# Kernel tuning notes

Hardware: AMD Instinct MI355X
Metric: run time of the kernel (lower is better)

The kernel has to match this reference:

```python
import jax, jax.numpy as jnp
import numpy as np

EPS = 1e-3  # keras LayerNormalization default epsilon


def layer_norm(x, g, b):
    mu = jnp.mean(x, axis=-1, keepdims=True)
    var = jnp.mean(jnp.square(x - mu), axis=-1, keepdims=True)
    return g * (x - mu) / jnp.sqrt(var + EPS) + b


def setup_inputs() -> dict:
    key = jax.random.key(0)
    ks = jax.random.split(key, 16)
    B, S, E, H, F = 2, 4096, 512, 8, 2048
    s_e = 1.0 / np.sqrt(E)
    s_f = 1.0 / np.sqrt(F)
    inp = {
        "x": jax.random.normal(ks[0], (B, S, E), dtype=jnp.float32),
        "WQ": jax.random.normal(ks[1], (E, E), dtype=jnp.float32) * s_e,
        "bQ": jnp.zeros((E,), jnp.float32),
        "WK": jax.random.normal(ks[2], (E, E), dtype=jnp.float32) * s_e,
        "bK": jnp.zeros((E,), jnp.float32),
        "WV": jax.random.normal(ks[3], (E, E), dtype=jnp.float32) * s_e,
        "bV": jnp.zeros((E,), jnp.float32),
        "WO": jax.random.normal(ks[4], (E, E), dtype=jnp.float32) * s_e,
        "bO": jnp.zeros((E,), jnp.float32),
        "W1": jax.random.normal(ks[5], (E, F), dtype=jnp.float32) * s_e,
        "b1": jnp.zeros((F,), jnp.float32),
        "W2": jax.random.normal(ks[6], (F, E), dtype=jnp.float32) * s_f,
        "b2": jnp.zeros((E,), jnp.float32),
        "g1": jnp.ones((E,), jnp.float32),
        "beta1": jnp.zeros((E,), jnp.float32),
        "g2": jnp.ones((E,), jnp.float32),
        "beta2": jnp.zeros((E,), jnp.float32),
        "num_head": 8,
    }
    return inp


def reference(x, WQ, bQ, WK, bK, WV, bV, WO, bO, W1, b1, W2, b2,
              g1, beta1, g2, beta2, num_head):
    B, S, E = x.shape
    H = num_head
    d = E // H
    scale = jnp.sqrt(jnp.asarray(d, jnp.float32))

    q = (x @ WQ + bQ).reshape(B, S, H, d).transpose(0, 2, 1, 3)  # [B,H,S,d]
    k = (x @ WK + bK).reshape(B, S, H, d).transpose(0, 2, 1, 3)
    v = (x @ WV + bV).reshape(B, S, H, d).transpose(0, 2, 1, 3)

    score = jnp.einsum('bhqd,bhkd->bhqk', q, k) / scale  # O(S^2) materialized, as in source
    attn = jax.nn.softmax(score, axis=-1)
    zs = jnp.einsum('bhqk,bhkd->bhqd', attn, v)  # [B,H,S,d]

    # Faithful to source bug: reshape [B,H,S,d] -> [B,S,E] WITHOUT transposing back
    zs = zs.reshape(B, S, E)
    zs = zs @ WO + bO

    z = layer_norm(zs + x, g1, beta1)
    r = jax.nn.relu(z @ W1 + b1) @ W2 + b2
    r = layer_norm(r + z, g2, beta2)
    return r
```

## Files before the change

### kernel.cpp

```cpp
#include <hip/hip_runtime.h>
#include <hip/hip_bf16.h>

typedef unsigned short u16;
typedef __attribute__((ext_vector_type(8))) short bf16x8;
typedef __attribute__((ext_vector_type(4))) float f32x4;
typedef __attribute__((ext_vector_type(16))) float f32x16;

static constexpr int BB = 2;
static constexpr int SS = 4096;
static constexpr int EE = 512;
static constexpr int HH = 8;
static constexpr int DD = 64;
static constexpr int FF = 2048;
static constexpr int NR = BB * SS;
static constexpr int QS = 3 * EE;

#define QSCALE 0.18033688011112042f

__device__ __forceinline__ u16 f2bf(float f) {
  union { float f; unsigned u; } v; v.f = f;
  unsigned r = v.u + 0x7FFFu + ((v.u >> 16) & 1u);
  return (u16)(r >> 16);
}
__device__ __forceinline__ unsigned pack2(float a, float b) {
  return (unsigned)f2bf(a) | ((unsigned)f2bf(b) << 16);
}
__device__ __forceinline__ unsigned cvtpk(float lo, float hi) {
  unsigned r;
  asm("v_cvt_pk_bf16_f32 %0, %1, %2" : "=v"(r) : "v"(lo), "v"(hi));
  return r;
}
__device__ __forceinline__ void perm32swap(unsigned& a, unsigned& b) {
  asm("v_permlane32_swap_b32 %0, %1" : "+v"(a), "+v"(b));
}
__device__ __forceinline__ void gload_lds16(const u16* g, u16* l) {
  __builtin_amdgcn_global_load_lds(
      (const __attribute__((address_space(1))) unsigned*)g,
      (__attribute__((address_space(3))) unsigned*)l, 16, 0, 0);
}

__global__ __launch_bounds__(256) void cvt_bf16(const float* __restrict__ x,
                                                u16* __restrict__ xb, int n) {
  int i = (blockIdx.x * 256 + threadIdx.x) * 8;
  if (i >= n) return;
  float4 a = *(const float4*)(x + i);
  float4 b = *(const float4*)(x + i + 4);
  uint4 u;
  u.x = pack2(a.x, a.y); u.y = pack2(a.z, a.w);
  u.z = pack2(b.x, b.y); u.w = pack2(b.z, b.w);
  *(uint4*)(xb + i) = u;
}

__global__ __launch_bounds__(256) void transp_bf16(const float* __restrict__ W,
                                                   u16* __restrict__ Wt,
                                                   int K, int N) {
  __shared__ float T[64][65];
  const int k0 = blockIdx.x * 64, n0 = blockIdx.y * 64;
  const int t = threadIdx.x;
  const int tn = t & 63, tk = t >> 6;
#pragma unroll
  for (int i = 0; i < 16; ++i) {
    int kk = tk * 16 + i;
    T[kk][tn] = W[(size_t)(k0 + kk) * N + n0 + tn];
  }
  __syncthreads();
#pragma unroll
  for (int i = 0; i < 16; ++i) {
    int nn = tk * 16 + i;
    Wt[(size_t)(n0 + nn) * K + k0 + tn] = f2bf(T[tn][nn]);
  }
}

__global__ __launch_bounds__(256) void transp_v(const u16* __restrict__ qkvb,
                                                u16* __restrict__ vt) {
  __shared__ u16 T[64][72];
  const int s0 = blockIdx.x * 64, c0 = blockIdx.y * 64, b = blockIdx.z;
  const int t = threadIdx.x;
#pragma unroll
  for (int i = 0; i < 2; ++i) {
    int idx = t + i * 256;
    int row = idx >> 3, c8 = idx & 7;
    *(uint4*)(&T[row][c8 * 8]) = *(const uint4*)(
        &qkvb[((size_t)b * SS + s0 + row) * QS + 1024 + c0 + c8 * 8]);
  }
  __syncthreads();
#pragma unroll
  for (int i = 0; i < 2; ++i) {
    int idx = t + i * 256;
    int c = idx >> 3, s8 = idx & 7;
    u16 tmp[8];
#pragma unroll
    for (int j = 0; j < 8; ++j) tmp[j] = T[s8 * 8 + j][c];
    *(uint4*)(&vt[((size_t)b * EE + c0 + c) * SS + s0 + s8 * 8]) =
        *(uint4*)tmp;
  }
}

__global__ void concat_bias(const float* __restrict__ bQ,
                            const float* __restrict__ bK,
                            const float* __restrict__ bV,
                            float* __restrict__ bqkv) {
  int i = blockIdx.x * 256 + threadIdx.x;
  if (i >= QS) return;
  bqkv[i] = i < 512 ? bQ[i] : (i < 1024 ? bK[i - 512] : bV[i - 1024]);
}

template <int RELU, int OUT_BF16, int SCALEQ = 0>
__global__ __launch_bounds__(256) void gemm_mfma(
    const u16* __restrict__ A, const u16* __restrict__ Bt,
    const float* __restrict__ bias, void* __restrict__ Cout,
    int M, int N, int K) {
  __shared__ __align__(16) u16 As[128 * 64];
  __shared__ __align__(16) u16 Bs[128 * 64];
  const int t = threadIdx.x;
  const int lane = t & 63, wid = t >> 6;
  const int lm = lane & 15, lg = lane >> 4;
  const int bm = blockIdx.x * 128, bn = blockIdx.y * 128;
  const int wr = (wid >> 1) * 64, wc = (wid & 1) * 64;
  const int sr = lane >> 3;
  const int scb = (lane & 7) ^ sr;

  f32x4 acc[4][4];
#pragma unroll
  for (int i = 0; i < 4; ++i)
#pragma unroll
    for (int j = 0; j < 4; ++j) acc[i][j] = (f32x4){0.f, 0.f, 0.f, 0.f};

  for (int kb = 0; kb < K; kb += 64) {
    __syncthreads();
#pragma unroll
    for (int i = 0; i < 4; ++i) {
      int rr = wid * 32 + i * 8 + sr;
      gload_lds16(A + (size_t)(bm + rr) * K + kb + scb * 8,
                  &As[(wid * 32 + i * 8) * 64]);
      gload_lds16(Bt + (size_t)(bn + rr) * K + kb + scb * 8,
                  &Bs[(wid * 32 + i * 8) * 64]);
    }
    __syncthreads();

#pragma unroll
    for (int c = 0; c < 2; ++c) {
      bf16x8 af[4], bfr[4];
#pragma unroll
      for (int i = 0; i < 4; ++i) {
        int ar = wr + i * 16 + lm;
        af[i] = *(const bf16x8*)(&As[ar * 64 + (((c * 4 + lg) ^ (ar & 7)) << 3)]);
        int br = wc + i * 16 + lm;
        bfr[i] = *(const bf16x8*)(&Bs[br * 64 + (((c * 4 + lg) ^ (br & 7)) << 3)]);
      }
#pragma unroll
      for (int i = 0; i < 4; ++i)
#pragma unroll
        for (int j = 0; j < 4; ++j)
          acc[i][j] = __builtin_amdgcn_mfma_f32_16x16x32_bf16(
              af[i], bfr[j], acc[i][j], 0, 0, 0);
    }
  }

  float bi[4];
#pragma unroll
  for (int j = 0; j < 4; ++j) bi[j] = bias[bn + wc + j * 16 + lm];

#pragma unroll
  for (int i = 0; i < 4; ++i) {
#pragma unroll
    for (int j = 0; j < 4; ++j) {
      int col = bn + wc + j * 16 + lm;
#pragma unroll
      for (int r = 0; r < 4; ++r) {
        int row = bm + wr + i * 16 + lg * 4 + r;
        float vv = acc[i][j][r] + bi[j];
        if (RELU) vv = fmaxf(vv, 0.f);
        if (SCALEQ && col < 512) vv *= QSCALE;
        if (OUT_BF16)
          ((u16*)Cout)[(size_t)row * N + col] = f2bf(vv);
        else
          ((float*)Cout)[(size_t)row * N + col] = vv;
      }
    }
  }
}

__global__ __launch_bounds__(128) void attn_mfma(
    const u16* __restrict__ qkv, const u16* __restrict__ vt,
    u16* __restrict__ zs) {
  __shared__ __align__(16) u16 K_lds[2][64 * 64];
  __shared__ __align__(16) u16 V_lds[2][64 * 64];
  __shared__ float Linv[2][32];

  const int qblock = blockIdx.x;
  const int bh = blockIdx.y;
  const int b = bh >> 3, h = bh & 7;
  const int t = threadIdx.x;
  const int lane = t & 63, wid = t >> 6;
  const int q32 = lane & 31, hi = lane >> 5;
  const int qs7 = q32 & 7;
  const size_t bS = (size_t)b * SS;
  const u16* kp = qkv + 512;
  const u16* vrow = vt + ((size_t)b * EE + h * DD) * SS;
  const int qbase = qblock * 64 + wid * 32;

  bf16x8 qf[4];
  {
    const u16* qrow = qkv + (bS + qbase + q32) * QS + h * DD + hi * 8;
#pragma unroll
    for (int c = 0; c < 4; ++c) qf[c] = *(const bf16x8*)(qrow + c * 16);
  }

  const int sr = lane >> 3;
  const int scb = (lane & 7) ^ sr;

  f32x16 o0, o1;
#pragma unroll
  for (int i = 0; i < 16; ++i) { o0[i] = 0.f; o1[i] = 0.f; }
  float lsum = 0.f;

  auto stage = [&](int kt, int bufi) {
#pragma unroll
    for (int i = 0; i < 4; ++i) {
      int rbase = wid * 32 + i * 8;
      gload_lds16(kp + (bS + kt * 64 + rbase + sr) * QS + h * DD + scb * 8,
                  &K_lds[bufi][rbase * 64]);
      gload_lds16(vrow + (size_t)(rbase + sr) * SS + kt * 64 + scb * 8,
                  &V_lds[bufi][rbase * 64]);
    }
  };

  stage(0, 0);

  for (int kt = 0; kt < SS / 64; ++kt) {
    const int cur = kt & 1;
    __syncthreads();
    if (kt + 1 < SS / 64) stage(kt + 1, cur ^ 1);

    float p[2][16];
#pragma unroll
    for (int blk = 0; blk < 2; ++blk) {
      f32x16 s;
#pragma unroll
      for (int i = 0; i < 16; ++i) s[i] = 0.f;
      const int krow = blk * 32 + q32;
      __builtin_amdgcn_s_setprio(1);
#pragma unroll
      for (int c = 0; c < 4; ++c) {
        bf16x8 kf = *(const bf16x8*)(
            &K_lds[cur][krow * 64 + (((2 * c + hi) ^ qs7) << 3)]);
        s = __builtin_amdgcn_mfma_f32_32x32x16_bf16(kf, qf[c], s, 0, 0, 0);
      }
      __builtin_amdgcn_s_setprio(0);
#pragma unroll
      for (int r = 0; r < 16; ++r) {
        p[blk][r] = __builtin_amdgcn_exp2f(s[r]);
        lsum += p[blk][r];
      }
    }

    __builtin_amdgcn_s_setprio(1);
#pragma unroll
    for (int kc = 0; kc < 4; ++kc) {
      const int bb = kc >> 1, rA = (kc & 1) * 8, rB = rA + 4;
      unsigned wA0 = cvtpk(p[bb][rA + 0], p[bb][rA + 1]);
      unsigned wA1 = cvtpk(p[bb][rA + 2], p[bb][rA + 3]);
      unsigned wB0 = cvtpk(p[bb][rB + 0], p[bb][rB + 1]);
      unsigned wB1 = cvtpk(p[bb][rB + 2], p[bb][rB + 3]);
      perm32swap(wA0, wB0);
      perm32swap(wA1, wB1);
      union { unsigned u[4]; bf16x8 v; } pf;
      pf.u[0] = wA0; pf.u[1] = wA1; pf.u[2] = wB0; pf.u[3] = wB1;
      bf16x8 vf0 = *(const bf16x8*)(
          &V_lds[cur][q32 * 64 + (((2 * kc + hi) ^ qs7) << 3)]);
      bf16x8 vf1 = *(const bf16x8*)(
          &V_lds[cur][(32 + q32) * 64 + (((2 * kc + hi) ^ qs7) << 3)]);
      o0 = __builtin_amdgcn_mfma_f32_32x32x16_bf16(pf.v, vf0, o0, 0, 0, 0);
      o1 = __builtin_amdgcn_mfma_f32_32x32x16_bf16(pf.v, vf1, o1, 0, 0, 0);
    }
    __builtin_amdgcn_s_setprio(0);
  }

  float fl = lsum + __shfl_xor(lsum, 32);
  if (lane < 32) Linv[wid][q32] = 1.f / fl;

#pragma unroll
  for (int reg = 0; reg < 16; ++reg) {
    int q = (reg & 3) + 8 * (reg >> 2) + 4 * hi;
    float inv = Linv[wid][q];
    int s = qbase + q;
    u16* dst = zs + ((size_t)b * SS + h * 512 + (s >> 3)) * EE + (s & 7) * 64;
    dst[q32] = f2bf(o0[reg] * inv);
    dst[32 + q32] = f2bf(o1[reg] * inv);
  }
}

template <int WB>
__global__ __launch_bounds__(128) void add_ln(
    const float* __restrict__ a, const float* __restrict__ xres,
    const float* __restrict__ g, const float* __restrict__ beta,
    float* __restrict__ outf, u16* __restrict__ outb) {
  const int row = blockIdx.x;
  const int tid = threadIdx.x;
  const float4 av = *(const float4*)(a + (size_t)row * EE + tid * 4);
  const float4 xv = *(const float4*)(xres + (size_t)row * EE + tid * 4);
  float vx = av.x + xv.x, vy = av.y + xv.y, vz = av.z + xv.z, vw = av.w + xv.w;
  float sum = vx + vy + vz + vw;
  float sq = vx * vx + vy * vy + vz * vz + vw * vw;
#pragma unroll
  for (int off = 1; off < 64; off <<= 1) {
    sum += __shfl_xor(sum, off);
    sq += __shfl_xor(sq, off);
  }
  __shared__ float s0[2], s1[2];
  int w = tid >> 6;
  if ((tid & 63) == 0) { s0[w] = sum; s1[w] = sq; }
  __syncthreads();
  sum = s0[0] + s0[1];
  sq = s1[0] + s1[1];
  float mu = sum * (1.0f / EE);
  float var = sq * (1.0f / EE) - mu * mu;
  float r = rsqrtf(var + 1e-3f);
  int c = tid * 4;
  float4 gv = *(const float4*)(g + c);
  float4 bv = *(const float4*)(beta + c);
  float4 ov;
  ov.x = gv.x * (vx - mu) * r + bv.x;
  ov.y = gv.y * (vy - mu) * r + bv.y;
  ov.z = gv.z * (vz - mu) * r + bv.z;
  ov.w = gv.w * (vw - mu) * r + bv.w;
  *(float4*)(outf + (size_t)row * EE + c) = ov;
  if (WB) {
    uint2 u;
    u.x = pack2(ov.x, ov.y);
    u.y = pack2(ov.z, ov.w);
    *(uint2*)(outb + (size_t)row * EE + c) = u;
  }
}

extern "C" void kernel_launch(void* const* d_in, const int* in_sizes, int n_in,
                              void* d_out, int out_size, void* d_ws,
                              size_t ws_size, hipStream_t stream) {
  const float* x = (const float*)d_in[0];
  const float* WQ = (const float*)d_in[1];
  const float* bQ = (const float*)d_in[2];
  const float* WK = (const float*)d_in[3];
  const float* bK = (const float*)d_in[4];
  const float* WV = (const float*)d_in[5];
  const float* bV = (const float*)d_in[6];
  const float* WO = (const float*)d_in[7];
  const float* bO = (const float*)d_in[8];
  const float* W1 = (const float*)d_in[9];
  const float* b1 = (const float*)d_in[10];
  const float* W2 = (const float*)d_in[11];
  const float* b2 = (const float*)d_in[12];
  const float* g1 = (const float*)d_in[13];
  const float* be1 = (const float*)d_in[14];
  const float* g2 = (const float*)d_in[15];
  const float* be2 = (const float*)d_in[16];
  float* out = (float*)d_out;

  const size_t MB = 1u << 20;
  char* w = (char*)d_ws;
  u16* Wqkv_t = (u16*)(w + 0);
  u16* WO_t   = (u16*)(w + 2 * MB);
  u16* W1_t   = (u16*)(w + 3 * MB);
  u16* W2_t   = (u16*)(w + 5 * MB);
  float* bqkv = (float*)(w + 7 * MB);
  u16* qkvb = (u16*)(w + 8 * MB);
  u16* zsb  = (u16*)(w + 32 * MB);
  float* zs2 = (float*)(w + 40 * MB);
  float* z   = (float*)(w + 56 * MB);
  u16* zb    = (u16*)(w + 72 * MB);
  u16* xb    = (u16*)(w + 80 * MB);
  u16* vtb   = (u16*)(w + 88 * MB);
  u16* f1    = (u16*)(w + 8 * MB);
  float* f2  = zs2;

  dim3 blk(256);

  cvt_bf16<<<dim3(NR * EE / 8 / 256), blk, 0, stream>>>(x, xb, NR * EE);
  transp_bf16<<<dim3(8, 8), blk, 0, stream>>>(WQ, Wqkv_t, EE, EE);
  transp_bf16<<<dim3(8, 8), blk, 0, stream>>>(WK, Wqkv_t + 512 * 512, EE, EE);
  transp_bf16<<<dim3(8, 8), blk, 0, stream>>>(WV, Wqkv_t + 1024 * 512, EE, EE);
  transp_bf16<<<dim3(8, 8), blk, 0, stream>>>(WO, WO_t, EE, EE);
  transp_bf16<<<dim3(8, 32), blk, 0, stream>>>(W1, W1_t, EE, FF);
  transp_bf16<<<dim3(32, 8), blk, 0, stream>>>(W2, W2_t, FF, EE);
  concat_bias<<<dim3(6), blk, 0, stream>>>(bQ, bK, bV, bqkv);

  gemm_mfma<0, 1, 1><<<dim3(64, 12), blk, 0, stream>>>(xb, Wqkv_t, bqkv, qkvb,
                                                       NR, QS, EE);
  transp_v<<<dim3(SS / 64, EE / 64, BB), blk, 0, stream>>>(qkvb, vtb);
  attn_mfma<<<dim3(SS / 64, BB * HH), dim3(128), 0, stream>>>(qkvb, vtb, zsb);
  gemm_mfma<0, 0><<<dim3(64, 4), blk, 0, stream>>>(zsb, WO_t, bO, zs2,
                                                   NR, EE, EE);
  add_ln<1><<<dim3(NR), dim3(128), 0, stream>>>(zs2, x, g1, be1, z, zb);
  gemm_mfma<1, 1><<<dim3(64, 16), blk, 0, stream>>>(zb, W1_t, b1, f1,
                                                    NR, FF, EE);
  gemm_mfma<0, 0><<<dim3(64, 4), blk, 0, stream>>>(f1, W2_t, b2, f2,
                                                   NR, EE, FF);
  add_ln<0><<<dim3(NR), dim3(128), 0, stream>>>(f2, z, g2, be2, out, nullptr);
}
```

Baseline: 257.2 us.

## Use 64x64 double-buffered GEMM tiles and fuse prep kernels into one launch

Replaces the 128x128 single-buffered MFMA GEMM with a 64x64 tile kernel that double-buffers LDS, issuing the next K-step's global-to-LDS loads before computing the current one. The grid grows fourfold, which gives the many CUs of the GPU more blocks, especially for the N=512 GEMMs that previously had only 256 blocks. Separately, the input conversion, the weight transposes and the bias concatenation are merged into a single prep kernel to cut launch overhead. The smaller tiles lower per-block operand reuse and increase global/L2 traffic per FLOP.

```diff
diff --git a/kernel.cpp b/kernel.cpp
--- a/kernel.cpp
+++ b/kernel.cpp
@@ -39,24 +39,11 @@
       (__attribute__((address_space(3))) unsigned*)l, 16, 0, 0);
 }
 
-__global__ __launch_bounds__(256) void cvt_bf16(const float* __restrict__ x,
-                                                u16* __restrict__ xb, int n) {
-  int i = (blockIdx.x * 256 + threadIdx.x) * 8;
-  if (i >= n) return;
-  float4 a = *(const float4*)(x + i);
-  float4 b = *(const float4*)(x + i + 4);
-  uint4 u;
-  u.x = pack2(a.x, a.y); u.y = pack2(a.z, a.w);
-  u.z = pack2(b.x, b.y); u.w = pack2(b.z, b.w);
-  *(uint4*)(xb + i) = u;
-}
-
-__global__ __launch_bounds__(256) void transp_bf16(const float* __restrict__ W,
-                                                   u16* __restrict__ Wt,
-                                                   int K, int N) {
+struct TrJob { const float* W; u16* Wt; int K, N, k0, n0; };
+
+__device__ __forceinline__ void transp_tile(const float* W, u16* Wt, int K,
+                                            int N, int k0, int n0, int t) {
   __shared__ float T[64][65];
-  const int k0 = blockIdx.x * 64, n0 = blockIdx.y * 64;
-  const int t = threadIdx.x;
   const int tn = t & 63, tk = t >> 6;
 #pragma unroll
   for (int i = 0; i < 16; ++i) {
@@ -69,6 +56,49 @@
     int nn = tk * 16 + i;
     Wt[(size_t)(n0 + nn) * K + k0 + tn] = f2bf(T[tn][nn]);
   }
+}
+
+__global__ __launch_bounds__(256) void prep_all(
+    const float* __restrict__ x, u16* __restrict__ xb,
+    const float* __restrict__ WQ, const float* __restrict__ WK,
+    const float* __restrict__ WV, const float* __restrict__ WO,
+    const float* __restrict__ W1, const float* __restrict__ W2,
+    u16* __restrict__ Wqkv_t, u16* __restrict__ WO_t, u16* __restrict__ W1_t,
+    u16* __restrict__ W2_t, const float* __restrict__ bQ,
+    const float* __restrict__ bK, const float* __restrict__ bV,
+    float* __restrict__ bqkv) {
+  const int bx = blockIdx.x;
+  const int t = threadIdx.x;
+  if (bx < 2048) {
+    int i = (bx * 256 + t) * 8;
+    float4 a = *(const float4*)(x + i);
+    float4 b = *(const float4*)(x + i + 4);
+    uint4 u;
+    u.x = pack2(a.x, a.y); u.y = pack2(a.z, a.w);
+    u.z = pack2(b.x, b.y); u.w = pack2(b.z, b.w);
+    *(uint4*)(xb + i) = u;
+    return;
+  }
+  int idx = bx - 2048;
+  if (idx < 768) {
+    TrJob j;
+    if (idx < 256) {
+      const float* srcs[4] = {WQ, WK, WV, WO};
+      u16* dsts[4] = {Wqkv_t, Wqkv_t + 512 * 512, Wqkv_t + 1024 * 512, WO_t};
+      int w = idx >> 6, l = idx & 63;
+      j = {srcs[w], dsts[w], 512, 512, (l & 7) * 64, (l >> 3) * 64};
+    } else if (idx < 512) {
+      int l = idx - 256;
+      j = {W1, W1_t, 512, 2048, (l & 7) * 64, (l >> 3) * 64};
+    } else {
+      int l = idx - 512;
+      j = {W2, W2_t, 2048, 512, (l & 31) * 64, (l >> 5) * 64};
+    }
+    transp_tile(j.W, j.Wt, j.K, j.N, j.k0, j.n0, t);
+    return;
+  }
+  for (int i = t; i < QS; i += 256)
+    bqkv[i] = i < 512 ? bQ[i] : (i < 1024 ? bK[i - 512] : bV[i - 1024]);
 }
 
 __global__ __launch_bounds__(256) void transp_v(const u16* __restrict__ qkvb,
@@ -96,75 +126,74 @@
   }
 }
 
-__global__ void concat_bias(const float* __restrict__ bQ,
-                            const float* __restrict__ bK,
-                            const float* __restrict__ bV,
-                            float* __restrict__ bqkv) {
-  int i = blockIdx.x * 256 + threadIdx.x;
-  if (i >= QS) return;
-  bqkv[i] = i < 512 ? bQ[i] : (i < 1024 ? bK[i - 512] : bV[i - 1024]);
-}
-
 template <int RELU, int OUT_BF16, int SCALEQ = 0>
-__global__ __launch_bounds__(256) void gemm_mfma(
+__global__ __launch_bounds__(256) void gemm64(
     const u16* __restrict__ A, const u16* __restrict__ Bt,
     const float* __restrict__ bias, void* __restrict__ Cout,
     int M, int N, int K) {
-  __shared__ __align__(16) u16 As[128 * 64];
-  __shared__ __align__(16) u16 Bs[128 * 64];
+  __shared__ __align__(16) u16 As[2][64 * 64];
+  __shared__ __align__(16) u16 Bs[2][64 * 64];
   const int t = threadIdx.x;
   const int lane = t & 63, wid = t >> 6;
   const int lm = lane & 15, lg = lane >> 4;
-  const int bm = blockIdx.x * 128, bn = blockIdx.y * 128;
-  const int wr = (wid >> 1) * 64, wc = (wid & 1) * 64;
+  const int bm = blockIdx.x * 64, bn = blockIdx.y * 64;
+  const int wr = (wid >> 1) * 32, wc = (wid & 1) * 32;
   const int sr = lane >> 3;
   const int scb = (lane & 7) ^ sr;
 
-  f32x4 acc[4][4];
-#pragma unroll
-  for (int i = 0; i < 4; ++i)
-#pragma unroll
-    for (int j = 0; j < 4; ++j) acc[i][j] = (f32x4){0.f, 0.f, 0.f, 0.f};
-
-  for (int kb = 0; kb < K; kb += 64) {
+  f32x4 acc[2][2];
+#pragma unroll
+  for (int i = 0; i < 2; ++i)
+#pragma unroll
+    for (int j = 0; j < 2; ++j) acc[i][j] = (f32x4){0.f, 0.f, 0.f, 0.f};
+
+  auto stage = [&](int kb, int buf) {
+#pragma unroll
+    for (int i = 0; i < 2; ++i) {
+      int r8 = wid * 16 + i * 8;
+      gload_lds16(A + (size_t)(bm + r8 + sr) * K + kb + scb * 8,
+                  &As[buf][r8 * 64]);
+      gload_lds16(Bt + (size_t)(bn + r8 + sr) * K + kb + scb * 8,
+                  &Bs[buf][r8 * 64]);
+    }
+  };
+
+  stage(0, 0);
+  const int nsteps = K >> 6;
+  for (int s = 0; s < nsteps; ++s) {
+    const int cur = s & 1;
     __syncthreads();
-#pragma unroll
-    for (int i = 0; i < 4; ++i) {
-      int rr = wid * 32 + i * 8 + sr;
-      gload_lds16(A + (size_t)(bm + rr) * K + kb + scb * 8,
-                  &As[(wid * 32 + i * 8) * 64]);
-      gload_lds16(Bt + (size_t)(bn + rr) * K + kb + scb * 8,
-                  &Bs[(wid * 32 + i * 8) * 64]);
-    }
-    __syncthreads();
+    if (s + 1 < nsteps) stage((s + 1) << 6, cur ^ 1);
 
 #pragma unroll
     for (int c = 0; c < 2; ++c) {
-      bf16x8 af[4], bfr[4];
-#pragma unroll
-      for (int i = 0; i < 4; ++i) {
+      bf16x8 af[2], bfr[2];
+#pragma unroll
+      for (int i = 0; i < 2; ++i) {
         int ar = wr + i * 16 + lm;
-        af[i] = *(const bf16x8*)(&As[ar * 64 + (((c * 4 + lg) ^ (ar & 7)) << 3)]);
+        af[i] = *(const bf16x8*)(
+            &As[cur][ar * 64 + (((c * 4 + lg) ^ (ar & 7)) << 3)]);
         int br = wc + i * 16 + lm;
-        bfr[i] = *(const bf16x8*)(&Bs[br * 64 + (((c * 4 + lg) ^ (br & 7)) << 3)]);
+        bfr[i] = *(const bf16x8*)(
+            &Bs[cur][br * 64 + (((c * 4 + lg) ^ (br & 7)) << 3)]);
       }
 #pragma unroll
-      for (int i = 0; i < 4; ++i)
-#pragma unroll
-        for (int j = 0; j < 4; ++j)
+      for (int i = 0; i < 2; ++i)
+#pragma unroll
+        for (int j = 0; j < 2; ++j)
           acc[i][j] = __builtin_amdgcn_mfma_f32_16x16x32_bf16(
               af[i], bfr[j], acc[i][j], 0, 0, 0);
     }
   }
 
-  float bi[4];
-#pragma unroll
-  for (int j = 0; j < 4; ++j) bi[j] = bias[bn + wc + j * 16 + lm];
-
-#pragma unroll
-  for (int i = 0; i < 4; ++i) {
-#pragma unroll
-    for (int j = 0; j < 4; ++j) {
+  float bi[2];
+#pragma unroll
+  for (int j = 0; j < 2; ++j) bi[j] = bias[bn + wc + j * 16 + lm];
+
+#pragma unroll
+  for (int i = 0; i < 2; ++i) {
+#pragma unroll
+    for (int j = 0; j < 2; ++j) {
       int col = bn + wc + j * 16 + lm;
 #pragma unroll
       for (int r = 0; r < 4; ++r) {
@@ -375,25 +404,20 @@
 
   dim3 blk(256);
 
-  cvt_bf16<<<dim3(NR * EE / 8 / 256), blk, 0, stream>>>(x, xb, NR * EE);
-  transp_bf16<<<dim3(8, 8), blk, 0, stream>>>(WQ, Wqkv_t, EE, EE);
-  transp_bf16<<<dim3(8, 8), blk, 0, stream>>>(WK, Wqkv_t + 512 * 512, EE, EE);
-  transp_bf16<<<dim3(8, 8), blk, 0, stream>>>(WV, Wqkv_t + 1024 * 512, EE, EE);
-  transp_bf16<<<dim3(8, 8), blk, 0, stream>>>(WO, WO_t, EE, EE);
-  transp_bf16<<<dim3(8, 32), blk, 0, stream>>>(W1, W1_t, EE, FF);
-  transp_bf16<<<dim3(32, 8), blk, 0, stream>>>(W2, W2_t, FF, EE);
-  concat_bias<<<dim3(6), blk, 0, stream>>>(bQ, bK, bV, bqkv);
-
-  gemm_mfma<0, 1, 1><<<dim3(64, 12), blk, 0, stream>>>(xb, Wqkv_t, bqkv, qkvb,
-                                                       NR, QS, EE);
+  prep_all<<<dim3(2817), blk, 0, stream>>>(x, xb, WQ, WK, WV, WO, W1, W2,
+                                           Wqkv_t, WO_t, W1_t, W2_t, bQ, bK,
+                                           bV, bqkv);
+
+  gemm64<0, 1, 1><<<dim3(128, 24), blk, 0, stream>>>(xb, Wqkv_t, bqkv, qkvb,
+                                                     NR, QS, EE);
   transp_v<<<dim3(SS / 64, EE / 64, BB), blk, 0, stream>>>(qkvb, vtb);
   attn_mfma<<<dim3(SS / 64, BB * HH), dim3(128), 0, stream>>>(qkvb, vtb, zsb);
-  gemm_mfma<0, 0><<<dim3(64, 4), blk, 0, stream>>>(zsb, WO_t, bO, zs2,
-                                                   NR, EE, EE);
+  gemm64<0, 0><<<dim3(128, 8), blk, 0, stream>>>(zsb, WO_t, bO, zs2,
+                                                 NR, EE, EE);
   add_ln<1><<<dim3(NR), dim3(128), 0, stream>>>(zs2, x, g1, be1, z, zb);
-  gemm_mfma<1, 1><<<dim3(64, 16), blk, 0, stream>>>(zb, W1_t, b1, f1,
-                                                    NR, FF, EE);
-  gemm_mfma<0, 0><<<dim3(64, 4), blk, 0, stream>>>(f1, W2_t, b2, f2,
-                                                   NR, EE, FF);
+  gemm64<1, 1><<<dim3(128, 32), blk, 0, stream>>>(zb, W1_t, b1, f1,
+                                                  NR, FF, EE);
+  gemm64<0, 0><<<dim3(128, 8), blk, 0, stream>>>(f1, W2_t, b2, f2,
+                                                 NR, EE, FF);
   add_ln<0><<<dim3(NR), dim3(128), 0, stream>>>(f2, z, g2, be2, out, nullptr);
 }
```

Result: faster. 231.2 us (-10.1%).
